# Optimization experiments

Measured on AMD Instinct MI355X. Metric: run time of the kernel, lower is better.

## Reference

```python
import jax, jax.numpy as jnp
import numpy as np

B, S, E, H = 2, 2048, 1024, 16
DH = E // H


def setup_inputs() -> dict:
    key = jax.random.key(0)
    ks = jax.random.split(key, 9)
    s = 1.0 / np.sqrt(E)
    return {
        "queries": jax.random.normal(ks[0], (B, S, E), dtype=jnp.float32),
        "keys": jax.random.normal(ks[1], (B, S, E), dtype=jnp.float32),
        "values": jax.random.normal(ks[2], (B, S, E), dtype=jnp.float32),
        "mask": jax.random.randint(ks[3], (B, 1, 1, S), 0, 2, dtype=jnp.int32),
        "Wq": jax.random.normal(ks[4], (E, E), dtype=jnp.float32) * s,
        "Wk": jax.random.normal(ks[5], (E, E), dtype=jnp.float32) * s,
        "Wv": jax.random.normal(ks[6], (E, E), dtype=jnp.float32) * s,
        "Wo": jax.random.normal(ks[7], (E, E), dtype=jnp.float32) * s,
        "bo": jax.random.normal(ks[8], (E,), dtype=jnp.float32) * s,
    }


def reference(queries, keys, values, mask, Wq, Wk, Wv, Wo, bo):
    n, d_q, _ = queries.shape
    d_k = keys.shape[1]
    # Linear projections (torch Linear: x @ W.T), then split into heads
    q = (queries @ Wq.T).reshape(n, d_q, H, DH)
    k = (keys @ Wk.T).reshape(n, d_k, H, DH)
    v = (values @ Wv.T).reshape(n, d_k, H, DH)
    # [n, H, d_q, d_k] attention scores
    energy = jnp.einsum("nqhd,nkhd->nhqk", q, k)
    energy = jnp.where(mask == 0, jnp.float32(-1e20), energy)
    # NOTE: original scales by sqrt(key seq length), not head dim -- kept faithful
    attn = jax.nn.softmax(energy / jnp.sqrt(jnp.float32(d_k)), axis=3)
    out = jnp.einsum("nhql,nlhd->nqhd", attn, v).reshape(n, d_q, E)
    return out @ Wo.T + bo
```

## Files before the change

### kernel.cpp

```cpp
#include <hip/hip_runtime.h>
#include <hip/hip_bf16.h>

#define BB 2
#define SS 2048
#define EE 1024
#define HH 16
#define DHH 64

using bf16x8 = __attribute__((ext_vector_type(8))) __bf16;
using f32x4  = __attribute__((ext_vector_type(4))) float;
using f32x16 = __attribute__((ext_vector_type(16))) float;
using uint2v = __attribute__((ext_vector_type(2))) unsigned int;

#if __has_builtin(__builtin_amdgcn_exp2f)
#define EXP2(x) __builtin_amdgcn_exp2f(x)
#else
#define EXP2(x) __exp2f(x)
#endif

__device__ int g_nkeep[2];

static __device__ __forceinline__ unsigned short f2bf(float f) {
    unsigned int u = __float_as_uint(f);
    u += 0x7FFFu + ((u >> 16) & 1u);
    return (unsigned short)(u >> 16);
}

static __device__ __forceinline__ unsigned int pk2bf(float lo, float hi) {
    union { __hip_bfloat162 h2; unsigned int u; } c;
    c.h2 = __float22bfloat162_rn(float2{lo, hi});
    return c.u;
}

static __device__ __forceinline__ void async_load16(const void* g, void* l) {
    __builtin_amdgcn_global_load_lds(
        (const __attribute__((address_space(1))) unsigned int*)g,
        (__attribute__((address_space(3))) unsigned int*)l, 16, 0, 0);
}

__global__ void cvt_kernel(const float* __restrict__ W0, const float* __restrict__ W1,
                           const float* __restrict__ W2, const float* __restrict__ W3,
                           const float* __restrict__ Xqs,
                           unsigned short* __restrict__ Wb,
                           unsigned short* __restrict__ Dq)
{
    const int z = blockIdx.y;
    const float* src;
    unsigned short* dst;
    if (z < 4) {
        if (blockIdx.x >= 512) return;
        src = (z == 0) ? W0 : (z == 1) ? W1 : (z == 2) ? W2 : W3;
        dst = Wb + (size_t)z * 1048576;
    } else {
        src = Xqs;
        dst = Dq;
    }
    const size_t base = (size_t)blockIdx.x * 2048 + (size_t)threadIdx.x * 8;
    const float4 f0 = *(const float4*)(src + base);
    const float4 f1 = *(const float4*)(src + base + 4);
    uint4 p;
    p.x = pk2bf(f0.x, f0.y); p.y = pk2bf(f0.z, f0.w);
    p.z = pk2bf(f1.x, f1.y); p.w = pk2bf(f1.z, f1.w);
    *(uint4*)(dst + base) = p;
}

__global__ __launch_bounds__(256, 2)
void gather_kernel(const float* __restrict__ Ksrc, const float* __restrict__ Vsrc,
                   const int* __restrict__ mask,
                   unsigned short* __restrict__ Xkc, unsigned short* __restrict__ Xvc)
{
    __shared__ int srcIdx[64];
    __shared__ int wsum[4];

    const int tid  = threadIdx.x;
    const int lane = tid & 63;
    const int wave = tid >> 6;
    const int b    = blockIdx.y;
    const int t0   = blockIdx.x * 64;
    const float* __restrict__ src = blockIdx.z ? Vsrc : Ksrc;
    unsigned short* __restrict__ dst = blockIdx.z ? Xvc : Xkc;

    const int base = tid * 8;
    int v[8]; int run = 0;
    #pragma unroll
    for (int i = 0; i < 8; i++) { v[i] = (mask[b * SS + base + i] != 0) ? 1 : 0; run += v[i]; }

    int inc = run;
    #pragma unroll
    for (int d = 1; d < 64; d <<= 1) {
        int n = __shfl_up(inc, d, 64);
        if (lane >= d) inc += n;
    }
    if (lane == 63) wsum[wave] = inc;
    __syncthreads();
    const int nkeep = wsum[0] + wsum[1] + wsum[2] + wsum[3];

    if (blockIdx.x == 0 && blockIdx.z == 0 && tid == 0) g_nkeep[b] = nkeep;

    if (t0 >= ((nkeep + 127) & ~127)) return;

    if (tid < 64) srcIdx[tid] = -1;
    __syncthreads();

    int r = inc - run;
    #pragma unroll
    for (int w = 0; w < 4; w++) if (w < wave) r += wsum[w];
    #pragma unroll
    for (int i = 0; i < 8; i++) {
        if (v[i]) {
            if (r >= t0 && r < t0 + 64) srcIdx[r - t0] = base + i;
            r++;
        }
    }
    __syncthreads();

    const int j = tid >> 2, part = tid & 3;
    const int s = srcIdx[j];
    unsigned short* drow = dst + ((size_t)(b * SS + t0 + j)) * EE + part * 256;
    if (s >= 0) {
        const float* srow = src + ((size_t)(b * SS + s)) * EE + part * 256;
        #pragma unroll
        for (int c = 0; c < 32; c++) {
            const float4 f0 = *(const float4*)(srow + c * 8);
            const float4 f1 = *(const float4*)(srow + c * 8 + 4);
            uint4 p;
            p.x = pk2bf(f0.x, f0.y); p.y = pk2bf(f0.z, f0.w);
            p.z = pk2bf(f1.x, f1.y); p.w = pk2bf(f1.z, f1.w);
            *(uint4*)(drow + c * 8) = p;
        }
    } else {
        #pragma unroll
        for (int c = 0; c < 32; c++) *(uint4*)(drow + c * 8) = uint4{0, 0, 0, 0};
    }
}

template<int MT, int NT, bool BF16OUT>
__global__ __launch_bounds__(256, 3)
void gemm_xwt(const unsigned short* __restrict__ X0, const unsigned short* __restrict__ X1,
              const unsigned short* __restrict__ X2,
              const unsigned short* __restrict__ W0, const unsigned short* __restrict__ W1,
              const unsigned short* __restrict__ W2,
              void* __restrict__ Y0, void* __restrict__ Y1, void* __restrict__ Y2,
              const float* __restrict__ bias, int M, int N, int K,
              float s0, float s1, float s2)
{
    constexpr int BK = 32;
    constexpr int NI = MT / 32;
    constexpr int NJ = NT / 32;
    constexpr int LPS = MT / 64 + NT / 64;
    __shared__ __align__(16) unsigned short As[3][MT * BK];
    __shared__ __align__(16) unsigned short Bs[3][NT * BK];

    const int z = blockIdx.z;
    const unsigned short* __restrict__ X = (z == 0) ? X0 : ((z == 1) ? X1 : X2);
    const unsigned short* __restrict__ W = (z == 0) ? W0 : ((z == 1) ? W1 : W2);
    void* __restrict__ Y                 = (z == 0) ? Y0 : ((z == 1) ? Y1 : Y2);
    const float ysc                      = (z == 0) ? s0 : ((z == 1) ? s1 : s2);

    const int tid  = threadIdx.x;
    const int lane = tid & 63;
    const int wave = tid >> 6;
    const int wm   = (wave >> 1) * (MT / 2);
    const int wn   = (wave & 1) * (NT / 2);

    const unsigned gx  = gridDim.x;
    const unsigned gy  = gridDim.y;
    const unsigned lin = blockIdx.x + gx * blockIdx.y;
    const unsigned k8  = lin & 7u;
    const unsigned j   = lin >> 3;
    const int m0 = (int)(k8 * (gy >> 3) + j / gx) * MT;
    const int n0 = (int)(j % gx) * NT;

    if (BF16OUT && z > 0) {
        const int bb = m0 >> 11;
        if ((m0 & 2047) >= g_nkeep[bb]) return;
    }

    const int l16  = lane & 15;
    const int quad = lane >> 4;

    const int arow = lane >> 2;
    const int akc  = ((lane & 3) ^ ((lane >> 3) & 3)) * 8;
    const int rchunk = (quad ^ ((l16 >> 1) & 3)) * 8;

    f32x4 acc[NI][NJ];
    #pragma unroll
    for (int i = 0; i < NI; i++)
        #pragma unroll
        for (int j2 = 0; j2 < NJ; j2++) acc[i][j2] = f32x4{0.f, 0.f, 0.f, 0.f};

    auto stage = [&](int k0, int buf) {
        #pragma unroll
        for (int j2 = 0; j2 < NT / 64; j2++) {
            const int rr = wave * (NT / 4) + j2 * 16;
            async_load16(W + (size_t)(n0 + rr + arow) * K + k0 + akc, Bs[buf] + rr * BK);
        }
        #pragma unroll
        for (int j2 = 0; j2 < MT / 64; j2++) {
            const int rr = wave * (MT / 4) + j2 * 16;
            async_load16(X + (size_t)(m0 + rr + arow) * K + k0 + akc, As[buf] + rr * BK);
        }
    };

    const int niter = K / BK;
    stage(0, 0);
    stage(BK, 1);
    int cur = 0;
    for (int i = 0; i < niter; i++) {
        if (i + 1 < niter) {
            if constexpr (LPS == 4) asm volatile("s_waitcnt vmcnt(4)" ::: "memory");
            else                    asm volatile("s_waitcnt vmcnt(3)" ::: "memory");
        } else {
            asm volatile("s_waitcnt vmcnt(0)" ::: "memory");
        }
        __builtin_amdgcn_s_barrier();
        if (i + 2 < niter) {
            const int nb = (cur >= 1) ? cur - 1 : 2;
            stage((i + 2) * BK, nb);
        }

        bf16x8 afrag[NI], bfrag[NJ];
        #pragma unroll
        for (int ii = 0; ii < NI; ii++)
            afrag[ii] = *(const bf16x8*)(As[cur] + (wm + ii * 16 + l16) * BK + rchunk);
        #pragma unroll
        for (int j2 = 0; j2 < NJ; j2++)
            bfrag[j2] = *(const bf16x8*)(Bs[cur] + (wn + j2 * 16 + l16) * BK + rchunk);
        #pragma unroll
        for (int ii = 0; ii < NI; ii++)
            #pragma unroll
            for (int j2 = 0; j2 < NJ; j2++)
                acc[ii][j2] = __builtin_amdgcn_mfma_f32_16x16x32_bf16(afrag[ii], bfrag[j2], acc[ii][j2], 0, 0, 0);

        cur = (cur < 2) ? cur + 1 : 0;
    }

    if (BF16OUT && z == 2) {
        #pragma unroll
        for (int i = 0; i < NI; i++) {
            #pragma unroll
            for (int j2 = 0; j2 < NJ; j2++) {
                const int row  = m0 + wm + i * 16 + quad * 4;
                const int bb   = row >> 11;
                const int slot = row & 2047;
                const int col  = n0 + wn + j2 * 16 + l16;
                uint2 pck;
                pck.x = pk2bf(acc[i][j2][0], acc[i][j2][1]);
                pck.y = pk2bf(acc[i][j2][2], acc[i][j2][3]);
                *(uint2*)((unsigned short*)Y + ((size_t)(bb * EE + col)) * SS + slot) = pck;
            }
        }
    } else {
        #pragma unroll
        for (int i = 0; i < NI; i++) {
            #pragma unroll
            for (int j2 = 0; j2 < NJ; j2++) {
                #pragma unroll
                for (int r = 0; r < 4; r++) {
                    const int row = m0 + wm + i * 16 + quad * 4 + r;
                    const int col = n0 + wn + j2 * 16 + l16;
                    const float v = acc[i][j2][r];
                    if (BF16OUT) {
                        ((unsigned short*)Y)[(size_t)row * N + col] = f2bf(v * ysc);
                    } else {
                        ((float*)Y)[(size_t)row * N + col] = v + bias[col];
                    }
                }
            }
        }
    }
}

__global__ __launch_bounds__(256, 2)
void attn_kernel(const unsigned short* __restrict__ Qb,
                 const unsigned short* __restrict__ Kc,
                 const unsigned short* __restrict__ Vtc,
                 const int* __restrict__ mask,
                 unsigned short* __restrict__ AO)
{
    constexpr int LDK = 68;
    constexpr int LDV = 68;
    __shared__ __align__(16) unsigned short Ks[64 * LDK];
    __shared__ __align__(16) unsigned short Vs[64 * LDV];
    __shared__ float Lsum[4][32];
    __shared__ int nk_s;

    const int tid  = threadIdx.x;
    const int lane = tid & 63;
    const int wave = tid >> 6;
    const int l32  = lane & 31;
    const int hi   = lane >> 5;

    const int linear = blockIdx.x;
    const int bh     = (linear & 7) * 4 + ((linear >> 3) & 3);
    const int qblk   = linear >> 5;
    const int b  = bh >> 4;
    const int h  = bh & 15;
    const int q0 = qblk * 128 + wave * 32;

    if (tid == 0) nk_s = 0;
    __syncthreads();
    {
        int cnt = 0;
        #pragma unroll
        for (int i = 0; i < 8; i++) cnt += (mask[b * SS + tid * 8 + i] != 0) ? 1 : 0;
        #pragma unroll
        for (int d = 32; d >= 1; d >>= 1) cnt += __shfl_xor(cnt, d, 64);
        if (lane == 0) atomicAdd(&nk_s, cnt);
    }
    __syncthreads();
    const int nkeep  = nk_s;
    const int ntiles = (nkeep + 63) >> 6;

    bf16x8 qf[4];
    {
        const unsigned short* qptr = Qb + (size_t)(b * SS + q0 + l32) * EE + h * DHH + hi * 8;
        #pragma unroll
        for (int t = 0; t < 4; t++) qf[t] = *(const bf16x8*)(qptr + t * 16);
    }

    float lsum = 0.f;
    f32x16 o_acc[2];
    #pragma unroll
    for (int d = 0; d < 2; d++)
        #pragma unroll
        for (int r = 0; r < 16; r++) o_acc[d][r] = 0.f;

    const int srow = tid >> 2;
    const int sc   = (tid & 3) * 16;

    uint4 kr0, kr1, vr0, vr1;
    auto gload = [&](int t0) {
        const unsigned short* kg = Kc + (size_t)(b * SS + t0 + srow) * EE + h * DHH + sc;
        kr0 = *(const uint4*)(kg);
        kr1 = *(const uint4*)(kg + 8);
        const unsigned short* vg = Vtc + (size_t)(b * EE + h * DHH + srow) * SS + t0 + sc;
        vr0 = *(const uint4*)(vg);
        vr1 = *(const uint4*)(vg + 8);
    };
    gload(0);

    for (int it = 0; it < ntiles; it++) {
        const int t0 = it * 64;
        __syncthreads();
        *(uint4*)(Ks + srow * LDK + sc)     = kr0;
        *(uint4*)(Ks + srow * LDK + sc + 8) = kr1;
        *(uint4*)(Vs + srow * LDV + sc)     = vr0;
        *(uint4*)(Vs + srow * LDV + sc + 8) = vr1;
        __syncthreads();

        if (it + 1 < ntiles) gload(t0 + 64);

        const bool full = (t0 + 64 <= nkeep);

        #pragma unroll
        for (int blk = 0; blk < 2; blk++) {
            f32x16 s;
            __builtin_amdgcn_s_setprio(1);
            {
                bf16x8 kf = *(const bf16x8*)(Ks + (blk * 32 + l32) * LDK + hi * 8);
                f32x16 z;
                #pragma unroll
                for (int r = 0; r < 16; r++) z[r] = 0.f;
                s = __builtin_amdgcn_mfma_f32_32x32x16_bf16(kf, qf[0], z, 0, 0, 0);
            }
            #pragma unroll
            for (int t = 1; t < 4; t++) {
                bf16x8 kf = *(const bf16x8*)(Ks + (blk * 32 + l32) * LDK + t * 16 + hi * 8);
                s = __builtin_amdgcn_mfma_f32_32x32x16_bf16(kf, qf[t], s, 0, 0, 0);
            }
            __builtin_amdgcn_s_setprio(0);

            float p[16];
            #pragma unroll
            for (int r = 0; r < 16; r++) p[r] = EXP2(s[r]);
            if (!full) {
                const int keyb = t0 + blk * 32 + 4 * hi;
                #pragma unroll
                for (int r = 0; r < 16; r++)
                    if (keyb + ((r & 3) + 8 * (r >> 2)) >= nkeep) p[r] = 0.f;
            }
            #pragma unroll
            for (int r = 0; r < 16; r += 4)
                lsum += ((p[r] + p[r + 1]) + (p[r + 2] + p[r + 3]));

            const unsigned int u0 = pk2bf(p[0],  p[1]);
            const unsigned int u1 = pk2bf(p[2],  p[3]);
            const unsigned int u2 = pk2bf(p[4],  p[5]);
            const unsigned int u3 = pk2bf(p[6],  p[7]);
            const unsigned int u4 = pk2bf(p[8],  p[9]);
            const unsigned int u5 = pk2bf(p[10], p[11]);
            const unsigned int u6 = pk2bf(p[12], p[13]);
            const unsigned int u7 = pk2bf(p[14], p[15]);
            const uint2v s02 = __builtin_amdgcn_permlane32_swap(u0, u2, false, false);
            const uint2v s13 = __builtin_amdgcn_permlane32_swap(u1, u3, false, false);
            const uint2v s46 = __builtin_amdgcn_permlane32_swap(u4, u6, false, false);
            const uint2v s57 = __builtin_amdgcn_permlane32_swap(u5, u7, false, false);

            union { unsigned int u[4]; bf16x8 v; } pa0, pa1;
            pa0.u[0] = s02.x; pa0.u[1] = s13.x; pa0.u[2] = s02.y; pa0.u[3] = s13.y;
            pa1.u[0] = s46.x; pa1.u[1] = s57.x; pa1.u[2] = s46.y; pa1.u[3] = s57.y;

            __builtin_amdgcn_s_setprio(1);
            #pragma unroll
            for (int kc = 0; kc < 2; kc++) {
                const bf16x8 pav = (kc == 0) ? pa0.v : pa1.v;
                #pragma unroll
                for (int dblk = 0; dblk < 2; dblk++) {
                    bf16x8 vf = *(const bf16x8*)(Vs + (dblk * 32 + l32) * LDV + blk * 32 + kc * 16 + hi * 8);
                    o_acc[dblk] = __builtin_amdgcn_mfma_f32_32x32x16_bf16(pav, vf, o_acc[dblk], 0, 0, 0);
                }
            }
            __builtin_amdgcn_s_setprio(0);
        }
    }

    {
        float ls = lsum;
        ls += __shfl_xor(ls, 32, 64);
        Lsum[wave][l32] = 1.0f / ls;
    }
    __builtin_amdgcn_s_waitcnt(0xC07F);

    #pragma unroll
    for (int r = 0; r < 16; r++) {
        const int qr = (r & 3) + 8 * (r >> 2) + 4 * hi;
        const float rl = Lsum[wave][qr];
        const size_t orow = (size_t)(b * SS + q0 + qr) * EE + h * DHH + l32;
        AO[orow]      = f2bf(o_acc[0][r] * rl);
        AO[orow + 32] = f2bf(o_acc[1][r] * rl);
    }
}

extern "C" void kernel_launch(void* const* d_in, const int* in_sizes, int n_in,
                              void* d_out, int out_size, void* d_ws, size_t ws_size,
                              hipStream_t stream)
{
    (void)in_sizes; (void)n_in; (void)out_size; (void)ws_size;
    const float* queries = (const float*)d_in[0];
    const float* keys    = (const float*)d_in[1];
    const float* values  = (const float*)d_in[2];
    const int*   mask    = (const int*)d_in[3];
    const float* Wq      = (const float*)d_in[4];
    const float* Wk      = (const float*)d_in[5];
    const float* Wv      = (const float*)d_in[6];
    const float* Wo      = (const float*)d_in[7];
    const float* bo      = (const float*)d_in[8];

    const size_t NE = (size_t)BB * SS * EE;
    const size_t WE = (size_t)EE * EE;

    unsigned short* Wb  = (unsigned short*)d_ws;
    unsigned short* Qb  = Wb + 4 * WE;
    unsigned short* Kc  = Qb + NE;
    unsigned short* Vtc = Kc + NE;
    unsigned short* Xvc = Vtc + NE;
    unsigned short* AOb = Xvc;

    unsigned short* Xq  = (unsigned short*)d_out;
    unsigned short* Xkc = Xq + NE;

    const int M = BB * SS, N = EE, K = EE;
    const float qscale = 0.022097086912079608f * 1.4426950408889634f;

    cvt_kernel<<<dim3(2048, 5), 256, 0, stream>>>(
        Wq, Wk, Wv, Wo, queries, Wb, Xq);

    gather_kernel<<<dim3(SS / 64, BB, 2), 256, 0, stream>>>(
        keys, values, mask, Xkc, Xvc);

    dim3 gproj(N / 128, M / 128, 3);
    gemm_xwt<128, 128, true><<<gproj, 256, 0, stream>>>(
        Xq, Xkc, Xvc, Wb, Wb + WE, Wb + 2 * WE,
        (void*)Qb, (void*)Kc, (void*)Vtc, nullptr, M, N, K,
        qscale, 1.0f, 1.0f);

    attn_kernel<<<dim3(512), 256, 0, stream>>>(Qb, Kc, Vtc, mask, AOb);

    dim3 gout(N / 64, M / 128, 1);
    gemm_xwt<128, 64, false><<<gout, 256, 0, stream>>>(
        AOb, AOb, AOb, Wb + 3 * WE, Wb + 3 * WE, Wb + 3 * WE,
        d_out, d_out, d_out, bo, M, N, K, 1.0f, 1.0f, 1.0f);
}
```

Before: 217.3 us.

## Fuse fp32-to-bf16 activation conversion and masked gather into projection GEMM

Drops the separate passes that converted queries to bf16 and gathered/converted masked key/value rows. The projection GEMM now reads fp32 activations through a per-row source-index table (built by the mask-scan blocks in the weight-conversion kernel), converts them in registers and writes them into swizzled LDS, with a two-stage register prefetch. This removes a full write and re-read of the bf16 activation copies and one kernel launch. In exchange the GEMM fetches twice as many A-operand bytes from global memory, and A loads now pass through registers instead of direct global-to-LDS copies, which adds register pressure and extra waits.

```diff
diff --git a/kernel.cpp b/kernel.cpp
--- a/kernel.cpp
+++ b/kernel.cpp
@@ -40,21 +40,51 @@
 
 __global__ void cvt_kernel(const float* __restrict__ W0, const float* __restrict__ W1,
                            const float* __restrict__ W2, const float* __restrict__ W3,
-                           const float* __restrict__ Xqs,
+                           const int* __restrict__ mask,
                            unsigned short* __restrict__ Wb,
-                           unsigned short* __restrict__ Dq)
+                           int* __restrict__ srcTab)
 {
     const int z = blockIdx.y;
-    const float* src;
-    unsigned short* dst;
-    if (z < 4) {
-        if (blockIdx.x >= 512) return;
-        src = (z == 0) ? W0 : (z == 1) ? W1 : (z == 2) ? W2 : W3;
-        dst = Wb + (size_t)z * 1048576;
-    } else {
-        src = Xqs;
-        dst = Dq;
-    }
+    if (z == 4) {
+        if (blockIdx.x >= 2) return;
+        __shared__ int wsum[4];
+        const int b    = blockIdx.x;
+        const int tid  = threadIdx.x;
+        const int lane = tid & 63;
+        const int wave = tid >> 6;
+
+        const int base = tid * 8;
+        int v[8]; int run = 0;
+        #pragma unroll
+        for (int i = 0; i < 8; i++) { v[i] = (mask[b * SS + base + i] != 0) ? 1 : 0; run += v[i]; }
+
+        int inc = run;
+        #pragma unroll
+        for (int d = 1; d < 64; d <<= 1) {
+            int n = __shfl_up(inc, d, 64);
+            if (lane >= d) inc += n;
+        }
+        if (lane == 63) wsum[wave] = inc;
+
+        #pragma unroll
+        for (int i = 0; i < 8; i++) srcTab[b * SS + base + i] = -1;
+        __syncthreads();
+
+        const int nkeep = wsum[0] + wsum[1] + wsum[2] + wsum[3];
+        if (tid == 0) g_nkeep[b] = nkeep;
+
+        int r = inc - run;
+        #pragma unroll
+        for (int w = 0; w < 4; w++) if (w < wave) r += wsum[w];
+        #pragma unroll
+        for (int i = 0; i < 8; i++) {
+            if (v[i]) { srcTab[b * SS + r] = base + i; r++; }
+        }
+        return;
+    }
+
+    const float* src = (z == 0) ? W0 : (z == 1) ? W1 : (z == 2) ? W2 : W3;
+    unsigned short* dst = Wb + (size_t)z * 1048576;
     const size_t base = (size_t)blockIdx.x * 2048 + (size_t)threadIdx.x * 8;
     const float4 f0 = *(const float4*)(src + base);
     const float4 f1 = *(const float4*)(src + base + 4);
@@ -64,80 +94,12 @@
     *(uint4*)(dst + base) = p;
 }
 
-__global__ __launch_bounds__(256, 2)
-void gather_kernel(const float* __restrict__ Ksrc, const float* __restrict__ Vsrc,
-                   const int* __restrict__ mask,
-                   unsigned short* __restrict__ Xkc, unsigned short* __restrict__ Xvc)
-{
-    __shared__ int srcIdx[64];
-    __shared__ int wsum[4];
-
-    const int tid  = threadIdx.x;
-    const int lane = tid & 63;
-    const int wave = tid >> 6;
-    const int b    = blockIdx.y;
-    const int t0   = blockIdx.x * 64;
-    const float* __restrict__ src = blockIdx.z ? Vsrc : Ksrc;
-    unsigned short* __restrict__ dst = blockIdx.z ? Xvc : Xkc;
-
-    const int base = tid * 8;
-    int v[8]; int run = 0;
-    #pragma unroll
-    for (int i = 0; i < 8; i++) { v[i] = (mask[b * SS + base + i] != 0) ? 1 : 0; run += v[i]; }
-
-    int inc = run;
-    #pragma unroll
-    for (int d = 1; d < 64; d <<= 1) {
-        int n = __shfl_up(inc, d, 64);
-        if (lane >= d) inc += n;
-    }
-    if (lane == 63) wsum[wave] = inc;
-    __syncthreads();
-    const int nkeep = wsum[0] + wsum[1] + wsum[2] + wsum[3];
-
-    if (blockIdx.x == 0 && blockIdx.z == 0 && tid == 0) g_nkeep[b] = nkeep;
-
-    if (t0 >= ((nkeep + 127) & ~127)) return;
-
-    if (tid < 64) srcIdx[tid] = -1;
-    __syncthreads();
-
-    int r = inc - run;
-    #pragma unroll
-    for (int w = 0; w < 4; w++) if (w < wave) r += wsum[w];
-    #pragma unroll
-    for (int i = 0; i < 8; i++) {
-        if (v[i]) {
-            if (r >= t0 && r < t0 + 64) srcIdx[r - t0] = base + i;
-            r++;
-        }
-    }
-    __syncthreads();
-
-    const int j = tid >> 2, part = tid & 3;
-    const int s = srcIdx[j];
-    unsigned short* drow = dst + ((size_t)(b * SS + t0 + j)) * EE + part * 256;
-    if (s >= 0) {
-        const float* srow = src + ((size_t)(b * SS + s)) * EE + part * 256;
-        #pragma unroll
-        for (int c = 0; c < 32; c++) {
-            const float4 f0 = *(const float4*)(srow + c * 8);
-            const float4 f1 = *(const float4*)(srow + c * 8 + 4);
-            uint4 p;
-            p.x = pk2bf(f0.x, f0.y); p.y = pk2bf(f0.z, f0.w);
-            p.z = pk2bf(f1.x, f1.y); p.w = pk2bf(f1.z, f1.w);
-            *(uint4*)(drow + c * 8) = p;
-        }
-    } else {
-        #pragma unroll
-        for (int c = 0; c < 32; c++) *(uint4*)(drow + c * 8) = uint4{0, 0, 0, 0};
-    }
-}
-
-template<int MT, int NT, bool BF16OUT>
+template<int MT, int NT, bool BF16OUT, int AMODE>
 __global__ __launch_bounds__(256, 3)
-void gemm_xwt(const unsigned short* __restrict__ X0, const unsigned short* __restrict__ X1,
-              const unsigned short* __restrict__ X2,
+void gemm_xwt(const unsigned short* __restrict__ Xb0, const unsigned short* __restrict__ Xb1,
+              const unsigned short* __restrict__ Xb2,
+              const float* __restrict__ Xf0, const float* __restrict__ Xf1,
+              const float* __restrict__ Xf2, const int* __restrict__ srcTab,
               const unsigned short* __restrict__ W0, const unsigned short* __restrict__ W1,
               const unsigned short* __restrict__ W2,
               void* __restrict__ Y0, void* __restrict__ Y1, void* __restrict__ Y2,
@@ -147,12 +109,10 @@
     constexpr int BK = 32;
     constexpr int NI = MT / 32;
     constexpr int NJ = NT / 32;
-    constexpr int LPS = MT / 64 + NT / 64;
     __shared__ __align__(16) unsigned short As[3][MT * BK];
     __shared__ __align__(16) unsigned short Bs[3][NT * BK];
 
     const int z = blockIdx.z;
-    const unsigned short* __restrict__ X = (z == 0) ? X0 : ((z == 1) ? X1 : X2);
     const unsigned short* __restrict__ W = (z == 0) ? W0 : ((z == 1) ? W1 : W2);
     void* __restrict__ Y                 = (z == 0) ? Y0 : ((z == 1) ? Y1 : Y2);
     const float ysc                      = (z == 0) ? s0 : ((z == 1) ? s1 : s2);
@@ -171,7 +131,7 @@
     const int m0 = (int)(k8 * (gy >> 3) + j / gx) * MT;
     const int n0 = (int)(j % gx) * NT;
 
-    if (BF16OUT && z > 0) {
+    if (AMODE == 1 && z > 0) {
         const int bb = m0 >> 11;
         if ((m0 & 2047) >= g_nkeep[bb]) return;
     }
@@ -182,6 +142,7 @@
     const int arow = lane >> 2;
     const int akc  = ((lane & 3) ^ ((lane >> 3) & 3)) * 8;
     const int rchunk = (quad ^ ((l16 >> 1) & 3)) * 8;
+    const int awc  = ((lane & 3) ^ ((arow >> 1) & 3)) * 8;
 
     f32x4 acc[NI][NJ];
     #pragma unroll
@@ -189,50 +150,117 @@
         #pragma unroll
         for (int j2 = 0; j2 < NJ; j2++) acc[i][j2] = f32x4{0.f, 0.f, 0.f, 0.f};
 
-    auto stage = [&](int k0, int buf) {
+    auto stageB = [&](int k0, int buf) {
         #pragma unroll
         for (int j2 = 0; j2 < NT / 64; j2++) {
             const int rr = wave * (NT / 4) + j2 * 16;
             async_load16(W + (size_t)(n0 + rr + arow) * K + k0 + akc, Bs[buf] + rr * BK);
         }
-        #pragma unroll
-        for (int j2 = 0; j2 < MT / 64; j2++) {
-            const int rr = wave * (MT / 4) + j2 * 16;
-            async_load16(X + (size_t)(m0 + rr + arow) * K + k0 + akc, As[buf] + rr * BK);
-        }
     };
 
-    const int niter = K / BK;
-    stage(0, 0);
-    stage(BK, 1);
-    int cur = 0;
-    for (int i = 0; i < niter; i++) {
-        if (i + 1 < niter) {
-            if constexpr (LPS == 4) asm volatile("s_waitcnt vmcnt(4)" ::: "memory");
-            else                    asm volatile("s_waitcnt vmcnt(3)" ::: "memory");
-        } else {
-            asm volatile("s_waitcnt vmcnt(0)" ::: "memory");
-        }
-        __builtin_amdgcn_s_barrier();
-        if (i + 2 < niter) {
-            const int nb = (cur >= 1) ? cur - 1 : 2;
-            stage((i + 2) * BK, nb);
-        }
-
+    auto compute = [&](int buf) {
         bf16x8 afrag[NI], bfrag[NJ];
         #pragma unroll
         for (int ii = 0; ii < NI; ii++)
-            afrag[ii] = *(const bf16x8*)(As[cur] + (wm + ii * 16 + l16) * BK + rchunk);
+            afrag[ii] = *(const bf16x8*)(As[buf] + (wm + ii * 16 + l16) * BK + rchunk);
         #pragma unroll
         for (int j2 = 0; j2 < NJ; j2++)
-            bfrag[j2] = *(const bf16x8*)(Bs[cur] + (wn + j2 * 16 + l16) * BK + rchunk);
+            bfrag[j2] = *(const bf16x8*)(Bs[buf] + (wn + j2 * 16 + l16) * BK + rchunk);
         #pragma unroll
         for (int ii = 0; ii < NI; ii++)
             #pragma unroll
             for (int j2 = 0; j2 < NJ; j2++)
                 acc[ii][j2] = __builtin_amdgcn_mfma_f32_16x16x32_bf16(afrag[ii], bfrag[j2], acc[ii][j2], 0, 0, 0);
-
-        cur = (cur < 2) ? cur + 1 : 0;
+    };
+
+    const int niter = K / BK;
+
+    if constexpr (AMODE == 0) {
+        const unsigned short* __restrict__ X = (z == 0) ? Xb0 : ((z == 1) ? Xb1 : Xb2);
+        auto stageA0 = [&](int k0, int buf) {
+            #pragma unroll
+            for (int j2 = 0; j2 < MT / 64; j2++) {
+                const int rr = wave * (MT / 4) + j2 * 16;
+                async_load16(X + (size_t)(m0 + rr + arow) * K + k0 + akc, As[buf] + rr * BK);
+            }
+        };
+        stageB(0, 0); stageA0(0, 0);
+        stageB(BK, 1); stageA0(BK, 1);
+        int cur = 0;
+        for (int i = 0; i < niter; i++) {
+            if (i + 1 < niter) {
+                asm volatile("s_waitcnt vmcnt(3)" ::: "memory");
+            } else {
+                asm volatile("s_waitcnt vmcnt(0)" ::: "memory");
+            }
+            __builtin_amdgcn_s_barrier();
+            if (i + 2 < niter) {
+                const int nb = (cur >= 1) ? cur - 1 : 2;
+                stageB((i + 2) * BK, nb); stageA0((i + 2) * BK, nb);
+            }
+            compute(cur);
+            cur = (cur < 2) ? cur + 1 : 0;
+        }
+    } else {
+        const float* __restrict__ XF = (z == 0) ? Xf0 : ((z == 1) ? Xf1 : Xf2);
+        const int bb   = m0 >> 11;
+        const int mloc = m0 & 2047;
+
+        const float* aptr[2];
+        bool azero[2];
+        #pragma unroll
+        for (int j2 = 0; j2 < 2; j2++) {
+            const int rloc = wave * (MT / 4) + j2 * 16 + arow;
+            int grow;
+            if (z == 0) {
+                grow = m0 + rloc; azero[j2] = false;
+            } else {
+                const int s = srcTab[bb * SS + mloc + rloc];
+                azero[j2] = (s < 0);
+                grow = bb * SS + (azero[j2] ? 0 : s);
+            }
+            aptr[j2] = XF + (size_t)grow * K + (lane & 3) * 8;
+        }
+
+        float4 aS0[4], aS1[4];
+        #define STAGE_A(k0, S)                                                \
+            { _Pragma("unroll")                                               \
+              for (int j2 = 0; j2 < 2; j2++) {                                \
+                  S[j2 * 2]     = *(const float4*)(aptr[j2] + (k0));          \
+                  S[j2 * 2 + 1] = *(const float4*)(aptr[j2] + (k0) + 4);      \
+              } }
+        #define WRITE_A(buf, S)                                               \
+            { _Pragma("unroll")                                               \
+              for (int j2 = 0; j2 < 2; j2++) {                                \
+                  uint4 w;                                                    \
+                  w.x = pk2bf(S[j2*2].x, S[j2*2].y);                          \
+                  w.y = pk2bf(S[j2*2].z, S[j2*2].w);                          \
+                  w.z = pk2bf(S[j2*2+1].x, S[j2*2+1].y);                      \
+                  w.w = pk2bf(S[j2*2+1].z, S[j2*2+1].w);                      \
+                  if (azero[j2]) w = uint4{0, 0, 0, 0};                       \
+                  const int rr = wave * (MT / 4) + j2 * 16 + arow;            \
+                  *(uint4*)(As[buf] + rr * BK + awc) = w;                     \
+              } }
+
+        stageB(0, 0);  STAGE_A(0, aS0);
+        stageB(BK, 1); STAGE_A(BK, aS1);
+        for (int i = 0; i < niter; i += 2) {
+            asm volatile("s_waitcnt vmcnt(6)" ::: "memory");
+            WRITE_A(i % 3, aS0);
+            asm volatile("s_waitcnt lgkmcnt(0)" ::: "memory");
+            __builtin_amdgcn_s_barrier();
+            if (i + 2 < niter) { stageB((i + 2) * BK, (i + 2) % 3); STAGE_A((i + 2) * BK, aS0); }
+            compute(i % 3);
+            if (i + 2 < niter) asm volatile("s_waitcnt vmcnt(6)" ::: "memory");
+            else               asm volatile("s_waitcnt vmcnt(0)" ::: "memory");
+            WRITE_A((i + 1) % 3, aS1);
+            asm volatile("s_waitcnt lgkmcnt(0)" ::: "memory");
+            __builtin_amdgcn_s_barrier();
+            if (i + 3 < niter) { stageB((i + 3) * BK, (i + 3) % 3); STAGE_A((i + 3) * BK, aS1); }
+            compute((i + 1) % 3);
+        }
+        #undef STAGE_A
+        #undef WRITE_A
     }
 
     if (BF16OUT && z == 2) {
@@ -241,13 +269,13 @@
             #pragma unroll
             for (int j2 = 0; j2 < NJ; j2++) {
                 const int row  = m0 + wm + i * 16 + quad * 4;
-                const int bb   = row >> 11;
+                const int bb2  = row >> 11;
                 const int slot = row & 2047;
                 const int col  = n0 + wn + j2 * 16 + l16;
                 uint2 pck;
                 pck.x = pk2bf(acc[i][j2][0], acc[i][j2][1]);
                 pck.y = pk2bf(acc[i][j2][2], acc[i][j2][3]);
-                *(uint2*)((unsigned short*)Y + ((size_t)(bb * EE + col)) * SS + slot) = pck;
+                *(uint2*)((unsigned short*)Y + ((size_t)(bb2 * EE + col)) * SS + slot) = pck;
             }
         }
     } else {
@@ -454,31 +482,30 @@
     unsigned short* Qb  = Wb + 4 * WE;
     unsigned short* Kc  = Qb + NE;
     unsigned short* Vtc = Kc + NE;
-    unsigned short* Xvc = Vtc + NE;
-    unsigned short* AOb = Xvc;
-
-    unsigned short* Xq  = (unsigned short*)d_out;
-    unsigned short* Xkc = Xq + NE;
+    unsigned short* AOb = Vtc + NE;
+
+    int* srcTab = (int*)d_out;
 
     const int M = BB * SS, N = EE, K = EE;
     const float qscale = 0.022097086912079608f * 1.4426950408889634f;
 
-    cvt_kernel<<<dim3(2048, 5), 256, 0, stream>>>(
-        Wq, Wk, Wv, Wo, queries, Wb, Xq);
-
-    gather_kernel<<<dim3(SS / 64, BB, 2), 256, 0, stream>>>(
-        keys, values, mask, Xkc, Xvc);
+    cvt_kernel<<<dim3(512, 5), 256, 0, stream>>>(
+        Wq, Wk, Wv, Wo, mask, Wb, srcTab);
 
     dim3 gproj(N / 128, M / 128, 3);
-    gemm_xwt<128, 128, true><<<gproj, 256, 0, stream>>>(
-        Xq, Xkc, Xvc, Wb, Wb + WE, Wb + 2 * WE,
+    gemm_xwt<128, 128, true, 1><<<gproj, 256, 0, stream>>>(
+        nullptr, nullptr, nullptr,
+        queries, keys, values, srcTab,
+        Wb, Wb + WE, Wb + 2 * WE,
         (void*)Qb, (void*)Kc, (void*)Vtc, nullptr, M, N, K,
         qscale, 1.0f, 1.0f);
 
     attn_kernel<<<dim3(512), 256, 0, stream>>>(Qb, Kc, Vtc, mask, AOb);
 
     dim3 gout(N / 64, M / 128, 1);
-    gemm_xwt<128, 64, false><<<gout, 256, 0, stream>>>(
-        AOb, AOb, AOb, Wb + 3 * WE, Wb + 3 * WE, Wb + 3 * WE,
+    gemm_xwt<128, 64, false, 0><<<gout, 256, 0, stream>>>(
+        AOb, AOb, AOb,
+        nullptr, nullptr, nullptr, nullptr,
+        Wb + 3 * WE, Wb + 3 * WE, Wb + 3 * WE,
         d_out, d_out, d_out, bo, M, N, K, 1.0f, 1.0f, 1.0f);
 }
```

New measurement: 205.1 us. -5.6%, faster.
